# Kernel optimization log

Measured on AMD Instinct MI355X. Metric: run time of the kernel, lower is better.

The kernel has to match this reference:

```python
import jax, jax.numpy as jnp
import numpy as np

VOXEL_SIZE = np.array([0.1, 0.1, 0.1], np.float32)
PC_MIN = np.array([-70.4, -40.0, -3.0], np.float32)
STRIDE = 8
NZ, NY, NX = 5, 100, 176          # dense voxel grid dims at this stride (z, y, x)
G = 6                             # ROI grid size
C_IN, C_MID = 64, 32              # backbone channels, per-point MLP widths
N_ROIS, N_VOX = 256, 30000
FC = 256

_o = np.arange(-1, 2)
OFFSETS = np.stack(np.meshgrid(_o, _o, _o, indexing='ij'), -1).reshape(-1, 3).astype(np.int32)  # (27,3) (dx,dy,dz)


def setup_inputs() -> dict:
    rng = np.random.default_rng(0)
    # rois: [x, y, z, dx, dy, dz, heading]
    ctr = np.stack([rng.uniform(-60, 60, N_ROIS), rng.uniform(-35, 35, N_ROIS), rng.uniform(-2.0, 0.5, N_ROIS)], -1)
    size = np.stack([rng.uniform(3.0, 5.0, N_ROIS), rng.uniform(1.5, 2.2, N_ROIS), rng.uniform(1.3, 1.9, N_ROIS)], -1)
    yaw = rng.uniform(-np.pi, np.pi, (N_ROIS, 1))
    rois = np.concatenate([ctr, size, yaw], -1).astype(np.float32)
    # unique sparse voxel coords stored as (x, y, z)
    flat = rng.choice(NZ * NY * NX, N_VOX, replace=False)
    z, y, x = np.unravel_index(flat, (NZ, NY, NX))
    voxel_coords = np.stack([x, y, z], -1).astype(np.int32)

    def W(*s):
        return jnp.asarray((rng.standard_normal(s) / np.sqrt(s[-1])).astype(np.float32))

    pre = G ** 3 * C_MID  # 6912, channel-major flattened pooled features
    return dict(
        rois=jnp.asarray(rois),
        voxel_features=jnp.asarray(rng.standard_normal((N_VOX, C_IN)).astype(np.float32)),
        voxel_coords=jnp.asarray(voxel_coords),
        w_mlp1=W(C_IN, C_MID), w_mlp2=W(C_MID, C_MID),
        w_fc1=W(FC, pre), w_fc2=W(FC, FC),
        w_cls1=W(FC, FC), w_cls2=W(FC, FC), w_cls3=W(1, FC), b_cls3=jnp.zeros((1,), jnp.float32),
        w_iou1=W(FC, FC), w_iou2=W(FC, FC), w_iou3=W(1, FC), b_iou3=jnp.zeros((1,), jnp.float32),
        w_reg1=W(FC, FC), w_reg2=W(FC, FC), w_reg3=W(7, FC) * 0.001, b_reg3=jnp.zeros((7,), jnp.float32),
    )


def _grid_points(rois):
    # dense GxGxG grid in each roi local frame, rotated by heading, shifted to center
    idx = jnp.stack(jnp.meshgrid(*([jnp.arange(G)] * 3), indexing='ij'), -1).reshape(-1, 3).astype(jnp.float32)
    size = rois[:, 3:6]                                               # (N,3)
    local = (idx[None] + 0.5) / G * size[:, None] - size[:, None] * 0.5  # (N,216,3)
    c, s = jnp.cos(rois[:, 6])[:, None], jnp.sin(rois[:, 6])[:, None]
    gx = local[..., 0] * c - local[..., 1] * s
    gy = local[..., 0] * s + local[..., 1] * c
    pts = jnp.stack([gx, gy, local[..., 2]], -1) + rois[:, None, 0:3]
    return pts.reshape(-1, 3)                                         # (N*G^3, 3)


def _build_v2p(voxel_coords, n_vox):
    v2p = jnp.full((NZ, NY, NX), -1, jnp.int32)
    return v2p.at[voxel_coords[:, 2], voxel_coords[:, 1], voxel_coords[:, 0]].set(
        jnp.arange(n_vox, dtype=jnp.int32))


def _forward(rois, voxel_features, v2p, w_mlp1, w_mlp2, w_fc1, w_fc2,
             w_cls1, w_cls2, w_cls3, b_cls3, w_iou1, w_iou2, w_iou3, b_iou3,
             w_reg1, w_reg2, w_reg3, b_reg3):
    xyz = _grid_points(rois)                                          # (M,3)
    coords = (jnp.floor((xyz - jnp.asarray(PC_MIN)) / jnp.asarray(VOXEL_SIZE)).astype(jnp.int32)) // STRIDE
    nc = coords[:, None, :] + jnp.asarray(OFFSETS)[None]              # (M,27,3) (x,y,z)
    lim = jnp.array([NX, NY, NZ], jnp.int32)
    valid = jnp.all((nc >= 0) & (nc < lim), axis=-1)
    ncl = jnp.clip(nc, 0, lim - 1)
    vidx = v2p[ncl[..., 2], ncl[..., 1], ncl[..., 0]]                 # (M,27) voxel index or -1
    valid = valid & (vidx >= 0)
    feat = voxel_features[jnp.clip(vidx, 0)]                          # (M,27,C_IN) irregular gather
    h = jax.nn.relu(feat @ w_mlp1)
    h = jax.nn.relu(h @ w_mlp2)                                       # (M,27,C_MID)
    pooled = jnp.max(jnp.where(valid[..., None], h, 0.0), axis=1)     # max-pool over neighbors
    n = rois.shape[0]
    # torch: (N, G^3, C) -> permute(0,2,1) -> view(N, C*G^3, 1): channel-major flatten
    flat = pooled.reshape(n, G ** 3, C_MID).transpose(0, 2, 1).reshape(n, -1)
    x = jax.nn.relu(flat @ w_fc1.T)
    x = jax.nn.relu(x @ w_fc2.T)

    def head(h1, h2, h3, b3):
        y = jax.nn.relu(x @ h1.T)
        y = jax.nn.relu(y @ h2.T)
        return y @ h3.T + b3

    rcnn_cls = head(w_cls1, w_cls2, w_cls3, b_cls3)   # (N,1)
    rcnn_iou = head(w_iou1, w_iou2, w_iou3, b_iou3)   # (N,1)
    rcnn_reg = head(w_reg1, w_reg2, w_reg3, b_reg3)   # (N,7)
    return rcnn_cls, rcnn_iou, rcnn_reg


def reference(rois, voxel_features, voxel_coords, w_mlp1, w_mlp2, w_fc1, w_fc2,
              w_cls1, w_cls2, w_cls3, b_cls3, w_iou1, w_iou2, w_iou3, b_iou3,
              w_reg1, w_reg2, w_reg3, b_reg3):
    v2p = _build_v2p(voxel_coords, voxel_features.shape[0])
    return _forward(rois, voxel_features, v2p, w_mlp1, w_mlp2, w_fc1, w_fc2,
                    w_cls1, w_cls2, w_cls3, b_cls3, w_iou1, w_iou2, w_iou3, b_iou3,
                    w_reg1, w_reg2, w_reg3, b_reg3)
```

## Files before the change

### kernel.cpp

```cpp
#include <hip/hip_runtime.h>

#define NZD 5
#define NYD 100
#define NXD 176
#define NVOX 30000
#define NROI 256
#define CIN 64
#define CMID 32
#define GPTS 216
#define KDIM 6912
#define PBLK 18
#define SPLITK 27


__global__ __launch_bounds__(256) void k_svmlp(const int* __restrict__ vc,
                                               const float* __restrict__ feat,
                                               const float* __restrict__ w1,
                                               const float* __restrict__ w2,
                                               int* __restrict__ v2p,
                                               float* __restrict__ h){
    __shared__ float W1[CIN*CMID];
    __shared__ float W2[CMID*CMID];
    int t = threadIdx.x;
    for (int i = t; i < CIN*CMID; i += 256) W1[i] = w1[i];
    for (int i = t; i < CMID*CMID; i += 256) W2[i] = w2[i];
    __syncthreads();
    int v = blockIdx.x*256 + t;
    if (v >= NVOX) return;
    int x = vc[v*3+0], y = vc[v*3+1], z = vc[v*3+2];
    v2p[(z*NYD + y)*NXD + x] = v;
    float h1[CMID];
    #pragma unroll
    for (int c = 0; c < CMID; ++c) h1[c] = 0.f;
    const float4* f4 = (const float4*)(feat + (size_t)v*CIN);
    #pragma unroll 4
    for (int k4 = 0; k4 < CIN/4; ++k4){
        float4 fv = f4[k4];
        int kb = k4*4;
        #pragma unroll
        for (int c = 0; c < CMID; ++c){
            h1[c] = fmaf(fv.x, W1[(kb+0)*CMID + c], h1[c]);
            h1[c] = fmaf(fv.y, W1[(kb+1)*CMID + c], h1[c]);
            h1[c] = fmaf(fv.z, W1[(kb+2)*CMID + c], h1[c]);
            h1[c] = fmaf(fv.w, W1[(kb+3)*CMID + c], h1[c]);
        }
    }
    #pragma unroll
    for (int c = 0; c < CMID; ++c) h1[c] = fmaxf(h1[c], 0.f);
    float h2[CMID];
    #pragma unroll
    for (int c = 0; c < CMID; ++c) h2[c] = 0.f;
    #pragma unroll 4
    for (int k = 0; k < CMID; ++k){
        float hv = h1[k];
        #pragma unroll
        for (int c = 0; c < CMID; ++c)
            h2[c] = fmaf(hv, W2[k*CMID + c], h2[c]);
    }
    float4* o4 = (float4*)(h + (size_t)v*CMID);
    #pragma unroll
    for (int q = 0; q < CMID/4; ++q)
        o4[q] = make_float4(fmaxf(h2[q*4+0],0.f), fmaxf(h2[q*4+1],0.f),
                            fmaxf(h2[q*4+2],0.f), fmaxf(h2[q*4+3],0.f));
}

__global__ __launch_bounds__(256) void k_pool(const float* __restrict__ rois,
                                              const int* __restrict__ v2p,
                                              const float* __restrict__ h,
                                              float* __restrict__ flat){
    __shared__ float P[PBLK*33];
    int r = blockIdx.y;
    int pbase = blockIdx.x * PBLK;
    int t = threadIdx.x;
    int g = t >> 5, lane = t & 31;
    float cx0 = rois[r*7+0], cy0 = rois[r*7+1], cz0 = rois[r*7+2];
    float dx  = rois[r*7+3], dy  = rois[r*7+4], dz  = rois[r*7+5];
    float yaw = rois[r*7+6];
    float cs = (float)cos((double)yaw);
    float sn = (float)sin((double)yaw);
    for (int pl = g; pl < PBLK; pl += 8){
        int p = pbase + pl;
        int i = p/36, j = (p/6)%6, k = p%6;
        int cX, cY, cZ;
        {
            #pragma clang fp contract(off)
            float lx = (((float)i + 0.5f)/6.0f)*dx - dx*0.5f;
            float ly = (((float)j + 0.5f)/6.0f)*dy - dy*0.5f;
            float lz = (((float)k + 0.5f)/6.0f)*dz - dz*0.5f;
            float gx = (lx*cs - ly*sn) + cx0;
            float gy = (lx*sn + ly*cs) + cy0;
            float gz = lz + cz0;
            float tx = (gx - (-70.4f)) / 0.1f;
            float ty = (gy - (-40.0f)) / 0.1f;
            float tz = (gz - (-3.0f))  / 0.1f;
            cX = ((int)floorf(tx)) >> 3;
            cY = ((int)floorf(ty)) >> 3;
            cZ = ((int)floorf(tz)) >> 3;
        }
        int vi[27];
        #pragma unroll
        for (int o = 0; o < 27; ++o){
            int ox = o % 3 - 1, oy = (o/3) % 3 - 1, oz = o/9 - 1;
            int nxc = cX+ox, nyc = cY+oy, nzc = cZ+oz;
            bool inb = ((unsigned)nxc < NXD) & ((unsigned)nyc < NYD) & ((unsigned)nzc < NZD);
            int cell = inb ? (nzc*NYD + nyc)*NXD + nxc : 0;
            int v = v2p[cell];
            vi[o] = inb ? v : -1;
        }
        float best = 0.f;
        #pragma unroll
        for (int o = 0; o < 27; ++o){
            if (vi[o] >= 0)
                best = fmaxf(best, h[(size_t)vi[o]*CMID + lane]);
        }
        P[pl*33 + lane] = best;
    }
    __syncthreads();
    for (int i2 = t; i2 < PBLK*CMID; i2 += 256){
        int pp = i2 % PBLK;
        int cc = i2 / PBLK;
        flat[(size_t)r*KDIM + cc*GPTS + pbase + pp] = P[pp*33 + cc];
    }
}

__global__ __launch_bounds__(256) void k_fc1(const float* __restrict__ A,
                                             const float* __restrict__ B,
                                             float* __restrict__ P){
    __shared__ float As[64][68];
    __shared__ float Bs[64][68];
    int t = threadIdx.x;
    int nb = blockIdx.x*64, mb = blockIdx.y*64, k0 = blockIdx.z*256;
    int tx = t & 15, ty = t >> 4;
    int lrow = t >> 4;
    int lcol = (t & 15)*4;
    float acc[4][4];
    #pragma unroll
    for (int i = 0; i < 4; ++i)
        #pragma unroll
        for (int j = 0; j < 4; ++j) acc[i][j] = 0.f;
    for (int kk = 0; kk < 4; ++kk){
        int ko = k0 + kk*64;
        #pragma unroll
        for (int it = 0; it < 4; ++it){
            int row = lrow + it*16;
            *(float4*)&As[row][lcol] = *(const float4*)&A[(size_t)(mb+row)*KDIM + ko + lcol];
            *(float4*)&Bs[row][lcol] = *(const float4*)&B[(size_t)(nb+row)*KDIM + ko + lcol];
        }
        __syncthreads();
        #pragma unroll 4
        for (int k4 = 0; k4 < 64; k4 += 4){
            float4 av[4], bv[4];
            #pragma unroll
            for (int i = 0; i < 4; ++i) av[i] = *(const float4*)&As[ty + 16*i][k4];
            #pragma unroll
            for (int j = 0; j < 4; ++j) bv[j] = *(const float4*)&Bs[tx + 16*j][k4];
            #pragma unroll
            for (int i = 0; i < 4; ++i)
                #pragma unroll
                for (int j = 0; j < 4; ++j){
                    acc[i][j] = fmaf(av[i].x, bv[j].x, acc[i][j]);
                    acc[i][j] = fmaf(av[i].y, bv[j].y, acc[i][j]);
                    acc[i][j] = fmaf(av[i].z, bv[j].z, acc[i][j]);
                    acc[i][j] = fmaf(av[i].w, bv[j].w, acc[i][j]);
                }
        }
        __syncthreads();
    }
    float* Pz = P + (size_t)blockIdx.z*65536;
    #pragma unroll
    for (int i = 0; i < 4; ++i)
        #pragma unroll
        for (int j = 0; j < 4; ++j)
            Pz[(size_t)(mb + ty + 16*i)*256 + nb + tx + 16*j] = acc[i][j];
}

__global__ __launch_bounds__(256) void k_tgemm(
    const float* __restrict__ A0, long strideA, int mode,
    const float* __restrict__ Wa, const float* __restrict__ Wb, const float* __restrict__ Wc,
    float* __restrict__ C0, long strideC)
{
    int z = blockIdx.z;
    const float* A = A0 + (size_t)z*strideA;
    const float* W = (z == 0) ? Wa : (z == 1) ? Wb : Wc;
    float* C = C0 + (size_t)z*strideC;
    __shared__ float As[32][68];
    __shared__ float Ws[32][68];
    int t = threadIdx.x;
    int nb = blockIdx.x*32, mb = blockIdx.y*32;
    int ty = t >> 4, tx = t & 15;
    float acc[2][2] = {{0.f,0.f},{0.f,0.f}};
    for (int kt = 0; kt < 4; ++kt){
        int ko = kt*64;
        #pragma unroll
        for (int it = 0; it < 2; ++it){
            int u = t + it*256;
            int row = u >> 4;
            int c4 = (u & 15) * 4;
            float4 av;
            if (mode == 2){
                const float* base = &A[(size_t)(mb+row)*256 + ko + c4];
                float4 s = make_float4(0.f,0.f,0.f,0.f);
                #pragma unroll
                for (int zz = 0; zz < SPLITK; ++zz){
                    float4 p = *(const float4*)&base[(size_t)zz*65536];
                    s.x += p.x; s.y += p.y; s.z += p.z; s.w += p.w;
                }
                av = make_float4(fmaxf(s.x,0.f), fmaxf(s.y,0.f),
                                 fmaxf(s.z,0.f), fmaxf(s.w,0.f));
            } else {
                av = *(const float4*)&A[(size_t)(mb+row)*256 + ko + c4];
            }
            *(float4*)&As[row][c4] = av;
            *(float4*)&Ws[row][c4] = *(const float4*)&W[(size_t)(nb+row)*256 + ko + c4];
        }
        __syncthreads();
        #pragma unroll
        for (int k4 = 0; k4 < 16; ++k4){
            float4 a0 = *(const float4*)&As[2*ty  ][k4*4];
            float4 a1 = *(const float4*)&As[2*ty+1][k4*4];
            float4 w0 = *(const float4*)&Ws[2*tx  ][k4*4];
            float4 w1 = *(const float4*)&Ws[2*tx+1][k4*4];
            acc[0][0]=fmaf(a0.x,w0.x,acc[0][0]); acc[0][0]=fmaf(a0.y,w0.y,acc[0][0]);
            acc[0][0]=fmaf(a0.z,w0.z,acc[0][0]); acc[0][0]=fmaf(a0.w,w0.w,acc[0][0]);
            acc[0][1]=fmaf(a0.x,w1.x,acc[0][1]); acc[0][1]=fmaf(a0.y,w1.y,acc[0][1]);
            acc[0][1]=fmaf(a0.z,w1.z,acc[0][1]); acc[0][1]=fmaf(a0.w,w1.w,acc[0][1]);
            acc[1][0]=fmaf(a1.x,w0.x,acc[1][0]); acc[1][0]=fmaf(a1.y,w0.y,acc[1][0]);
            acc[1][0]=fmaf(a1.z,w0.z,acc[1][0]); acc[1][0]=fmaf(a1.w,w0.w,acc[1][0]);
            acc[1][1]=fmaf(a1.x,w1.x,acc[1][1]); acc[1][1]=fmaf(a1.y,w1.y,acc[1][1]);
            acc[1][1]=fmaf(a1.z,w1.z,acc[1][1]); acc[1][1]=fmaf(a1.w,w1.w,acc[1][1]);
        }
        __syncthreads();
    }
    #pragma unroll
    for (int i = 0; i < 2; ++i)
        #pragma unroll
        for (int j = 0; j < 2; ++j)
            C[(size_t)(mb+2*ty+i)*256 + nb+2*tx+j] = fmaxf(acc[i][j], 0.f);
}

__global__ __launch_bounds__(256) void k_final(const float* __restrict__ y2,
    const float* __restrict__ wc3, const float* __restrict__ bc3,
    const float* __restrict__ wi3, const float* __restrict__ bi3,
    const float* __restrict__ wr3, const float* __restrict__ br3,
    float* __restrict__ out){
    __shared__ float red[4];
    int r = blockIdx.x, t = threadIdx.x;
    auto reduce_out = [&](float v, float bias, int idx){
        #pragma unroll
        for (int off = 32; off > 0; off >>= 1) v += __shfl_down(v, off);
        if ((t & 63) == 0) red[t >> 6] = v;
        __syncthreads();
        if (t == 0) out[idx] = red[0] + red[1] + red[2] + red[3] + bias;
        __syncthreads();
    };
    float yc = y2[(size_t)r*256 + t];
    float yi = y2[65536 + (size_t)r*256 + t];
    float yr = y2[131072 + (size_t)r*256 + t];
    reduce_out(yc*wc3[t], bc3[0], r);
    reduce_out(yi*wi3[t], bi3[0], 256 + r);
    for (int q = 0; q < 7; ++q)
        reduce_out(yr*wr3[q*256 + t], br3[q], 512 + r*7 + q);
}

extern "C" void kernel_launch(void* const* d_in, const int* in_sizes, int n_in,
                              void* d_out, int out_size, void* d_ws, size_t ws_size,
                              hipStream_t stream){
    const float* rois  = (const float*)d_in[0];
    const float* vfeat = (const float*)d_in[1];
    const int*   vcrd  = (const int*)d_in[2];
    const float* wm1   = (const float*)d_in[3];
    const float* wm2   = (const float*)d_in[4];
    const float* wfc1  = (const float*)d_in[5];
    const float* wfc2  = (const float*)d_in[6];
    const float* wc1   = (const float*)d_in[7];
    const float* wc2   = (const float*)d_in[8];
    const float* wc3   = (const float*)d_in[9];
    const float* bc3   = (const float*)d_in[10];
    const float* wi1   = (const float*)d_in[11];
    const float* wi2   = (const float*)d_in[12];
    const float* wi3   = (const float*)d_in[13];
    const float* bi3   = (const float*)d_in[14];
    const float* wr1   = (const float*)d_in[15];
    const float* wr2   = (const float*)d_in[16];
    const float* wr3   = (const float*)d_in[17];
    const float* br3   = (const float*)d_in[18];
    float* out = (float*)d_out;

    char* ws = (char*)d_ws;
    int*   v2p   = (int*)(ws + 0);
    float* h     = (float*)(ws + 352256);
    float* flat  = (float*)(ws + 4192512);
    float* x2    = (float*)(ws + 11270656);
    float* y1    = (float*)(ws + 11532800);
    float* y2    = (float*)(ws + 12319232);
    float* parts = (float*)(ws + 13105664);

    k_svmlp  <<<dim3(118),      dim3(256), 0, stream>>>(vcrd, vfeat, wm1, wm2, v2p, h);
    k_pool   <<<dim3(12, 256),  dim3(256), 0, stream>>>(rois, v2p, h, flat);
    k_fc1    <<<dim3(4,4,SPLITK), dim3(256), 0, stream>>>(flat, wfc1, parts);
    k_tgemm  <<<dim3(8,8,1),    dim3(256), 0, stream>>>(parts, 0,  2, wfc2, wfc2, wfc2, x2, 0);
    k_tgemm  <<<dim3(8,8,3),    dim3(256), 0, stream>>>(x2, 0,     0, wc1,  wi1,  wr1,  y1, 65536);
    k_tgemm  <<<dim3(8,8,3),    dim3(256), 0, stream>>>(y1, 65536, 0, wc2,  wi2,  wr2,  y2, 65536);
    k_final  <<<dim3(256),      dim3(256), 0, stream>>>(y2, wc3, bc3, wi3, bi3, wr3, br3, out);
}
```

Before: 215.5 us.

## Fuse split-K reduce, fc2, all three heads and projections into one kernel

Replaces the three tiled GEMM launches and the final projection kernel with a single kernel where each block owns two ROIs and runs fc2, the three two-layer heads and the output projections from shared memory. This removes four launches and the global round-trips for the intermediate activations. In exchange, each of the 128 blocks streams every 256x256 weight matrix (seven layers) from global or L2, with a sync-heavy single-accumulator inner loop and low parallelism.

```diff
diff --git a/kernel.cpp b/kernel.cpp
--- a/kernel.cpp
+++ b/kernel.cpp
@@ -174,92 +174,89 @@
             Pz[(size_t)(mb + ty + 16*i)*256 + nb + tx + 16*j] = acc[i][j];
 }
 
-__global__ __launch_bounds__(256) void k_tgemm(
-    const float* __restrict__ A0, long strideA, int mode,
-    const float* __restrict__ Wa, const float* __restrict__ Wb, const float* __restrict__ Wc,
-    float* __restrict__ C0, long strideC)
+__global__ __launch_bounds__(256) void k_tail2(const float* __restrict__ parts,
+    const float* __restrict__ wfc2,
+    const float* __restrict__ wc1, const float* __restrict__ wc2,
+    const float* __restrict__ wc3, const float* __restrict__ bc3,
+    const float* __restrict__ wi1, const float* __restrict__ wi2,
+    const float* __restrict__ wi3, const float* __restrict__ bi3,
+    const float* __restrict__ wr1, const float* __restrict__ wr2,
+    const float* __restrict__ wr3, const float* __restrict__ br3,
+    float* __restrict__ out)
 {
-    int z = blockIdx.z;
-    const float* A = A0 + (size_t)z*strideA;
-    const float* W = (z == 0) ? Wa : (z == 1) ? Wb : Wc;
-    float* C = C0 + (size_t)z*strideC;
-    __shared__ float As[32][68];
-    __shared__ float Ws[32][68];
-    int t = threadIdx.x;
-    int nb = blockIdx.x*32, mb = blockIdx.y*32;
-    int ty = t >> 4, tx = t & 15;
-    float acc[2][2] = {{0.f,0.f},{0.f,0.f}};
-    for (int kt = 0; kt < 4; ++kt){
-        int ko = kt*64;
-        #pragma unroll
-        for (int it = 0; it < 2; ++it){
-            int u = t + it*256;
-            int row = u >> 4;
-            int c4 = (u & 15) * 4;
-            float4 av;
-            if (mode == 2){
-                const float* base = &A[(size_t)(mb+row)*256 + ko + c4];
-                float4 s = make_float4(0.f,0.f,0.f,0.f);
+    __shared__ float Ab[2][260];
+    __shared__ float Xb[2][260];
+    __shared__ float Yb[2][260];
+    __shared__ float Zb[2][260];
+    __shared__ float Ws[128][68];
+    __shared__ float red[4];
+    int t = threadIdx.x;
+    int m0 = blockIdx.x * 2;
+
+    #pragma unroll
+    for (int e = 0; e < 2; ++e){
+        int idx = e*256 + t;
+        int m = idx >> 8, c = idx & 255;
+        float s = 0.f;
+        #pragma unroll
+        for (int zz = 0; zz < SPLITK; ++zz)
+            s += parts[(size_t)zz*65536 + (size_t)(m0+m)*256 + c];
+        Ab[m][c] = fmaxf(s, 0.f);
+    }
+    __syncthreads();
+
+    auto layer = [&](float (*S)[260], const float* __restrict__ W, float (*D)[260]){
+        int m = t >> 7;
+        int n = t & 127;
+        int r0 = t >> 4;
+        int c4 = (t & 15) * 4;
+        #pragma unroll
+        for (int nb = 0; nb < 2; ++nb){
+            float acc = 0.f;
+            for (int kt = 0; kt < 4; ++kt){
                 #pragma unroll
-                for (int zz = 0; zz < SPLITK; ++zz){
-                    float4 p = *(const float4*)&base[(size_t)zz*65536];
-                    s.x += p.x; s.y += p.y; s.z += p.z; s.w += p.w;
+                for (int it = 0; it < 8; ++it){
+                    int row = r0 + it*16;
+                    *(float4*)&Ws[row][c4] =
+                        *(const float4*)&W[(size_t)(nb*128 + row)*256 + kt*64 + c4];
                 }
-                av = make_float4(fmaxf(s.x,0.f), fmaxf(s.y,0.f),
-                                 fmaxf(s.z,0.f), fmaxf(s.w,0.f));
-            } else {
-                av = *(const float4*)&A[(size_t)(mb+row)*256 + ko + c4];
+                __syncthreads();
+                #pragma unroll
+                for (int k4 = 0; k4 < 16; ++k4){
+                    float4 wv = *(const float4*)&Ws[n][k4*4];
+                    float4 av = *(const float4*)&S[m][kt*64 + k4*4];
+                    acc = fmaf(av.x, wv.x, acc);
+                    acc = fmaf(av.y, wv.y, acc);
+                    acc = fmaf(av.z, wv.z, acc);
+                    acc = fmaf(av.w, wv.w, acc);
+                }
+                __syncthreads();
             }
-            *(float4*)&As[row][c4] = av;
-            *(float4*)&Ws[row][c4] = *(const float4*)&W[(size_t)(nb+row)*256 + ko + c4];
-        }
-        __syncthreads();
-        #pragma unroll
-        for (int k4 = 0; k4 < 16; ++k4){
-            float4 a0 = *(const float4*)&As[2*ty  ][k4*4];
-            float4 a1 = *(const float4*)&As[2*ty+1][k4*4];
-            float4 w0 = *(const float4*)&Ws[2*tx  ][k4*4];
-            float4 w1 = *(const float4*)&Ws[2*tx+1][k4*4];
-            acc[0][0]=fmaf(a0.x,w0.x,acc[0][0]); acc[0][0]=fmaf(a0.y,w0.y,acc[0][0]);
-            acc[0][0]=fmaf(a0.z,w0.z,acc[0][0]); acc[0][0]=fmaf(a0.w,w0.w,acc[0][0]);
-            acc[0][1]=fmaf(a0.x,w1.x,acc[0][1]); acc[0][1]=fmaf(a0.y,w1.y,acc[0][1]);
-            acc[0][1]=fmaf(a0.z,w1.z,acc[0][1]); acc[0][1]=fmaf(a0.w,w1.w,acc[0][1]);
-            acc[1][0]=fmaf(a1.x,w0.x,acc[1][0]); acc[1][0]=fmaf(a1.y,w0.y,acc[1][0]);
-            acc[1][0]=fmaf(a1.z,w0.z,acc[1][0]); acc[1][0]=fmaf(a1.w,w0.w,acc[1][0]);
-            acc[1][1]=fmaf(a1.x,w1.x,acc[1][1]); acc[1][1]=fmaf(a1.y,w1.y,acc[1][1]);
-            acc[1][1]=fmaf(a1.z,w1.z,acc[1][1]); acc[1][1]=fmaf(a1.w,w1.w,acc[1][1]);
-        }
-        __syncthreads();
-    }
-    #pragma unroll
-    for (int i = 0; i < 2; ++i)
-        #pragma unroll
-        for (int j = 0; j < 2; ++j)
-            C[(size_t)(mb+2*ty+i)*256 + nb+2*tx+j] = fmaxf(acc[i][j], 0.f);
-}
-
-__global__ __launch_bounds__(256) void k_final(const float* __restrict__ y2,
-    const float* __restrict__ wc3, const float* __restrict__ bc3,
-    const float* __restrict__ wi3, const float* __restrict__ bi3,
-    const float* __restrict__ wr3, const float* __restrict__ br3,
-    float* __restrict__ out){
-    __shared__ float red[4];
-    int r = blockIdx.x, t = threadIdx.x;
-    auto reduce_out = [&](float v, float bias, int idx){
-        #pragma unroll
-        for (int off = 32; off > 0; off >>= 1) v += __shfl_down(v, off);
-        if ((t & 63) == 0) red[t >> 6] = v;
-        __syncthreads();
-        if (t == 0) out[idx] = red[0] + red[1] + red[2] + red[3] + bias;
+            D[m][nb*128 + n] = fmaxf(acc, 0.f);
+        }
         __syncthreads();
     };
-    float yc = y2[(size_t)r*256 + t];
-    float yi = y2[65536 + (size_t)r*256 + t];
-    float yr = y2[131072 + (size_t)r*256 + t];
-    reduce_out(yc*wc3[t], bc3[0], r);
-    reduce_out(yi*wi3[t], bi3[0], 256 + r);
-    for (int q = 0; q < 7; ++q)
-        reduce_out(yr*wr3[q*256 + t], br3[q], 512 + r*7 + q);
+
+    auto project = [&](float (*S)[260], const float* __restrict__ w3,
+                       const float* __restrict__ b3, int nq, int outbase, int qstride){
+        int m = t >> 7;
+        int c = t & 127;
+        for (int q = 0; q < nq; ++q){
+            float v = S[m][c] * w3[q*256 + c] + S[m][c+128] * w3[q*256 + c + 128];
+            #pragma unroll
+            for (int off = 32; off > 0; off >>= 1) v += __shfl_down(v, off);
+            if ((t & 63) == 0) red[t >> 6] = v;
+            __syncthreads();
+            if (t < 2)
+                out[outbase + (m0 + t)*qstride + q] = red[t*2] + red[t*2+1] + b3[q];
+            __syncthreads();
+        }
+    };
+
+    layer(Ab, wfc2, Xb);
+    layer(Xb, wc1, Yb); layer(Yb, wc2, Zb); project(Zb, wc3, bc3, 1, 0,   1);
+    layer(Xb, wi1, Yb); layer(Yb, wi2, Zb); project(Zb, wi3, bi3, 1, 256, 1);
+    layer(Xb, wr1, Yb); layer(Yb, wr2, Zb); project(Zb, wr3, br3, 7, 512, 7);
 }
 
 extern "C" void kernel_launch(void* const* d_in, const int* in_sizes, int n_in,
@@ -290,16 +287,13 @@
     int*   v2p   = (int*)(ws + 0);
     float* h     = (float*)(ws + 352256);
     float* flat  = (float*)(ws + 4192512);
-    float* x2    = (float*)(ws + 11270656);
-    float* y1    = (float*)(ws + 11532800);
-    float* y2    = (float*)(ws + 12319232);
     float* parts = (float*)(ws + 13105664);
 
-    k_svmlp  <<<dim3(118),      dim3(256), 0, stream>>>(vcrd, vfeat, wm1, wm2, v2p, h);
-    k_pool   <<<dim3(12, 256),  dim3(256), 0, stream>>>(rois, v2p, h, flat);
+    k_svmlp  <<<dim3(118),        dim3(256), 0, stream>>>(vcrd, vfeat, wm1, wm2, v2p, h);
+    k_pool   <<<dim3(12, 256),    dim3(256), 0, stream>>>(rois, v2p, h, flat);
     k_fc1    <<<dim3(4,4,SPLITK), dim3(256), 0, stream>>>(flat, wfc1, parts);
-    k_tgemm  <<<dim3(8,8,1),    dim3(256), 0, stream>>>(parts, 0,  2, wfc2, wfc2, wfc2, x2, 0);
-    k_tgemm  <<<dim3(8,8,3),    dim3(256), 0, stream>>>(x2, 0,     0, wc1,  wi1,  wr1,  y1, 65536);
-    k_tgemm  <<<dim3(8,8,3),    dim3(256), 0, stream>>>(y1, 65536, 0, wc2,  wi2,  wr2,  y2, 65536);
-    k_final  <<<dim3(256),      dim3(256), 0, stream>>>(y2, wc3, bc3, wi3, bi3, wr3, br3, out);
-}
+    k_tail2  <<<dim3(128),        dim3(256), 0, stream>>>(parts, wfc2,
+                                                          wc1, wc2, wc3, bc3,
+                                                          wi1, wi2, wi3, bi3,
+                                                          wr1, wr2, wr3, br3, out);
+}
```

Result: slower. 224.5 us (+4.2%).
